# Performance work log

Measured on AMD Instinct MI355X. Metric: run time of the kernel, lower is better.

The kernel has to match this reference:

```python
import jax, jax.numpy as jnp
import numpy as np

B_GR = 128    # graphs per batch
N0 = 512      # nodes per graph before pooling
E_PER = 4096  # edges per graph (kept static; pooled-away edges get weight 0)
H = 128       # hidden
F = 128       # num_features (== hidden)
C = 10        # num_classes
K_HOP = 3     # Jacobi polynomial order (hop_num)
A_J, B_J = 1.0, 1.0
EPS = 1e-5


def _bn(h, g, b):
    # training-mode BatchNorm1d: batch stats, biased variance
    m = jnp.mean(h, 0)
    v = jnp.mean((h - m) ** 2, 0)
    return (h - m) * jax.lax.rsqrt(v + EPS) * g + b


def _forward(x, convW, convb, bnW, bnB, bn7W, bn7B, attW, theta,
             lin1W, lin1b, lin2W, lin2b, lin3W, lin3b, src, dst):
    w = jnp.ones((src.shape[0],), x.dtype)  # edge weights; 0 => filtered edge
    n = N0
    h = x
    reads = []
    for i in range(5):
        N = B_GR * n
        # symmetric GCN normalization with self loops on the weighted graph
        deg = jax.ops.segment_sum(w, dst, num_segments=N) + 1.0
        dinv = jax.lax.rsqrt(deg)
        enorm = dinv[src] * dinv[dst] * w   # per-edge norm [E]
        snorm = dinv * dinv                 # self-loop norm [N]
        prop = lambda m_: jax.ops.segment_sum(enorm[:, None] * m_[src], dst, num_segments=N) + m_ * snorm[:, None]
        pvec = lambda v_: jax.ops.segment_sum(enorm * v_[src], dst, num_segments=N) + v_ * snorm
        # GCNConv -> BN -> ReLU
        h = prop(h @ convW[i]) + convb[i]
        h = jax.nn.relu(_bn(h, bnW[i], bnB[i]))
        # JacobiPool: Jacobi-polynomial diffusion of attention scores
        s0 = h @ attW[i]                    # [N]
        polys = [s0, 0.5 * ((A_J - B_J) * s0 + (A_J + B_J + 2.0) * pvec(s0))]
        for kk in range(2, K_HOP + 1):
            c0 = 2 * kk * (kk + A_J + B_J) * (2 * kk + A_J + B_J - 2)
            c1 = (2 * kk + A_J + B_J - 1) * (2 * kk + A_J + B_J) * (2 * kk + A_J + B_J - 2)
            c2 = (2 * kk + A_J + B_J - 1) * (A_J * A_J - B_J * B_J)
            c3 = 2 * (kk + A_J - 1) * (kk + B_J - 1) * (2 * kk + A_J + B_J)
            polys.append((c1 * pvec(polys[-1]) + c2 * polys[-1] - c3 * polys[-2]) / c0)
        score = sum(theta[i, j] * polys[j] for j in range(K_HOP + 1))
        # top-k node selection per graph (ratio 0.5 -> static k)
        k = n // 2
        _, idx = jax.lax.top_k(score.reshape(B_GR, n), k)
        sel = (idx + (jnp.arange(B_GR) * n)[:, None]).reshape(-1)  # global node ids [B*k]
        h = h[sel] * jnp.tanh(score[sel])[:, None]
        # remap/filter edges to surviving nodes (masked, static edge count)
        new_id = jnp.full((N,), -1, jnp.int32).at[sel].set(jnp.arange(B_GR * k, dtype=jnp.int32))
        ns, nd = new_id[src], new_id[dst]
        valid = (ns >= 0) & (nd >= 0) & (w > 0)
        w = valid.astype(x.dtype)
        src = jnp.where(valid, ns, 0)
        dst = jnp.where(valid, nd, 0)
        # readout: global max pool || global mean pool per graph
        xg = h.reshape(B_GR, k, H)
        reads.append(jnp.concatenate([xg.max(1), xg.mean(1)], -1))
        n = k
    g = sum(reads) / 5.0                    # [B, 2H]
    g = jax.nn.relu(_bn(g @ lin1W + lin1b, bnW[5], bnB[5]))
    g = jax.nn.relu(_bn(g @ lin2W + lin2b, bn7W, bn7B))
    return jax.nn.log_softmax(g @ lin3W + lin3b, -1)


def setup_inputs() -> dict:
    key = jax.random.key(0)
    ks = jax.random.split(key, 8)
    N = B_GR * N0
    E = B_GR * E_PER
    rng = np.random.default_rng(0)
    off = np.repeat(np.arange(B_GR, dtype=np.int32) * N0, E_PER)
    src = jnp.asarray(off + rng.integers(0, N0, E).astype(np.int32))
    dst = jnp.asarray(off + rng.integers(0, N0, E).astype(np.int32))
    s = 1.0 / np.sqrt(H)
    return {
        "x": jax.random.normal(ks[0], (N, F), jnp.float32),
        "convW": jax.random.normal(ks[1], (5, H, H), jnp.float32) * s,
        "convb": jnp.zeros((5, H), jnp.float32),
        "bnW": jnp.ones((6, H), jnp.float32),
        "bnB": jnp.zeros((6, H), jnp.float32),
        "bn7W": jnp.ones((H // 2,), jnp.float32),
        "bn7B": jnp.zeros((H // 2,), jnp.float32),
        "attW": jax.random.normal(ks[2], (5, H), jnp.float32) * s,
        "theta": jax.random.normal(ks[3], (5, K_HOP + 1), jnp.float32) * 0.5,
        "lin1W": jax.random.normal(ks[4], (2 * H, H), jnp.float32) * (1.0 / np.sqrt(2 * H)),
        "lin1b": jnp.zeros((H,), jnp.float32),
        "lin2W": jax.random.normal(ks[5], (H, H // 2), jnp.float32) * s,
        "lin2b": jnp.zeros((H // 2,), jnp.float32),
        "lin3W": jax.random.normal(ks[6], (H // 2, C), jnp.float32) * (1.0 / np.sqrt(H // 2)),
        "lin3b": jnp.zeros((C,), jnp.float32),
        "src": src,
        "dst": dst,
    }


def reference(x, convW, convb, bnW, bnB, bn7W, bn7B, attW, theta,
              lin1W, lin1b, lin2W, lin2b, lin3W, lin3b, src, dst):
    return _forward(x, convW, convb, bnW, bnB, bn7W, bn7B, attW, theta,
                    lin1W, lin1b, lin2W, lin2b, lin3W, lin3b, src, dst)
```

## Files before the change

kernel.cpp:

```cpp
#include <hip/hip_runtime.h>
#include <hip/hip_bf16.h>

#define B_GRAPH 128
#define ETOT    (128*4096)
#define N0G     (128*512)
#define HF      128
#define STSZ    2048

union IGSmem {
    float Ws[64*HF];
    struct { int cnt[512]; int cur[512]; float dvl[512]; } ini;
};

__global__ __launch_bounds__(256) void k_init_gemm(
    const float* __restrict__ A, const float* __restrict__ Wg, float* __restrict__ C,
    const int* __restrict__ s_in, const int* __restrict__ d_in_,
    int* __restrict__ srcw, int* __restrict__ dstw, float* __restrict__ wv,
    int2* __restrict__ csr, int2* __restrict__ rb2, float* __restrict__ dinvv,
    float* __restrict__ gacc, float* __restrict__ statsH,
    float* __restrict__ st0, float* __restrict__ st1, float* __restrict__ st2)
{
    __shared__ IGSmem sm;
    int t = threadIdx.x;
    if (blockIdx.x < 1024){
        int tx = t & 15, ty = t >> 4;
        int r0 = blockIdx.x*64 + ty*4, c0 = tx*4;
        float acc[4][8];
        #pragma unroll
        for (int j=0;j<4;++j)
            #pragma unroll
            for (int l=0;l<8;++l) acc[j][l] = 0.f;
        for (int kh = 0; kh < 2; ++kh){
            __syncthreads();
            {
                float4* d4 = (float4*)sm.Ws;
                const float4* s4 = (const float4*)(Wg + kh*64*HF);
                for (int i = t; i < 64*HF/4; i += 256) d4[i] = s4[i];
            }
            __syncthreads();
            for (int k4 = 0; k4 < 16; ++k4){
                float4 av[4];
                #pragma unroll
                for (int j=0;j<4;++j)
                    av[j] = *(const float4*)(A + (size_t)(r0+j)*HF + kh*64 + k4*4);
                #pragma unroll
                for (int kk=0; kk<4; ++kk){
                    int kl = k4*4 + kk;
                    float4 w0 = *(const float4*)(sm.Ws + kl*HF + c0);
                    float4 w1 = *(const float4*)(sm.Ws + kl*HF + c0 + 64);
                    #pragma unroll
                    for (int j=0;j<4;++j){
                        float a = reinterpret_cast<const float*>(&av[j])[kk];
                        acc[j][0] += a*w0.x; acc[j][1] += a*w0.y; acc[j][2] += a*w0.z; acc[j][3] += a*w0.w;
                        acc[j][4] += a*w1.x; acc[j][5] += a*w1.y; acc[j][6] += a*w1.z; acc[j][7] += a*w1.w;
                    }
                }
            }
        }
        #pragma unroll
        for (int j=0;j<4;++j){
            *(float4*)(C + (size_t)(r0+j)*HF + c0)      = make_float4(acc[j][0],acc[j][1],acc[j][2],acc[j][3]);
            *(float4*)(C + (size_t)(r0+j)*HF + c0 + 64) = make_float4(acc[j][4],acc[j][5],acc[j][6],acc[j][7]);
        }
    } else {
        int g = blockIdx.x - 1024;
        for (int l = t; l < 512; l += 256) sm.ini.cnt[l] = 0;
        gacc[g*256 + t] = 0.f;
        if (g == 0){
            if (t < 256){ statsH[t] = 0.f; if (t < 128) statsH[256+t] = 0.f; }
            for (int i = t; i < STSZ; i += 256){ st0[i] = 0.f; st1[i] = 0.f; st2[i] = 0.f; }
        }
        __syncthreads();
        for (int j = t; j < 4096; j += 256){
            int e = g*4096 + j;
            int sg = s_in[e], dg = d_in_[e];
            srcw[e] = sg; dstw[e] = dg; wv[e] = 1.f;
            atomicAdd(&sm.ini.cnt[dg & 511], 1);
        }
        __syncthreads();
        int c0 = sm.ini.cnt[2*t], c1 = sm.ini.cnt[2*t+1];
        int pairsum = c0 + c1;
        sm.ini.cur[t] = pairsum;
        __syncthreads();
        for (int off = 1; off < 256; off <<= 1){
            int a = (t >= off) ? sm.ini.cur[t-off] : 0;
            __syncthreads();
            sm.ini.cur[t] += a;
            __syncthreads();
        }
        int begpair = sm.ini.cur[t] - pairsum;
        __syncthreads();
        sm.ini.cur[2*t]   = begpair;
        sm.ini.cur[2*t+1] = begpair + c0;
        __syncthreads();
        for (int l = t; l < 512; l += 256){
            rb2[g*512 + l] = make_int2(g*4096 + sm.ini.cur[l], sm.ini.cnt[l]);
            float dv = rsqrtf((float)sm.ini.cnt[l] + 1.f);
            sm.ini.dvl[l] = dv;
            dinvv[g*512 + l] = dv;
        }
        __syncthreads();
        for (int j = t; j < 4096; j += 256){
            int e = g*4096 + j;
            int sg = srcw[e], dl = dstw[e] & 511;
            int p = atomicAdd(&sm.ini.cur[dl], 1);
            csr[g*4096 + p] = make_int2(sg, __float_as_int(sm.ini.dvl[sg & 511]));
        }
    }
}

__global__ __launch_bounds__(256) void k_prop_stats(const float* __restrict__ Y, const float* __restrict__ cb,
                                                    const int2* __restrict__ rb2, const int2* __restrict__ cp,
                                                    const float* __restrict__ dinv,
                                                    float* __restrict__ X, float* __restrict__ st,
                                                    int n, int lb, int Nn){
    __shared__ float rs[1024], rq[1024];
    int xcd = blockIdx.x & 7, c = blockIdx.x >> 3;
    int g = xcd*16 + (c >> lb);
    int m = c & ((1 << lb) - 1);
    int nd = threadIdx.x >> 5;
    int v = g*n + m*8 + nd;
    int f4 = threadIdx.x & 31;
    float dv = dinv[v];
    float4 y = *(const float4*)(Y + (size_t)v*HF + f4*4);
    float4 acc = make_float4(0.f, 0.f, 0.f, 0.f);
    int2 rb = rb2[v];
    int e0 = rb.x, e1 = rb.x + rb.y;
    for (int j = e0; j < e1; ++j){
        int2 e = cp[j];
        int s = e.x & (Nn - 1);
        float en = __int_as_float(e.y);
        float4 h = *(const float4*)(Y + (size_t)s*HF + f4*4);
        acc.x += en*h.x; acc.y += en*h.y; acc.z += en*h.z; acc.w += en*h.w;
    }
    int f = f4*4;
    acc.x = y.x*dv*dv + dv*acc.x + cb[f];
    acc.y = y.y*dv*dv + dv*acc.y + cb[f+1];
    acc.z = y.z*dv*dv + dv*acc.z + cb[f+2];
    acc.w = y.w*dv*dv + dv*acc.w + cb[f+3];
    *(float4*)(X + (size_t)v*HF + f) = acc;
    *(float4*)&rs[nd*HF + f] = acc;
    *(float4*)&rq[nd*HF + f] = make_float4(acc.x*acc.x, acc.y*acc.y, acc.z*acc.z, acc.w*acc.w);
    __syncthreads();
    if (threadIdx.x < 128){
        int tt = threadIdx.x;
        float s = 0.f, q = 0.f;
        #pragma unroll
        for (int j = 0; j < 8; ++j){ s += rs[j*HF + tt]; q += rq[j*HF + tt]; }
        atomicAdd(&st[xcd*256 + tt], s);
        atomicAdd(&st[xcd*256 + 128 + tt], q);
    }
}

union __align__(16) KSmem {
    struct {
        int2  eds[4096]; int2 rbl[512];
        float dvv[512], p0[512], p1[512], p2[512];
        float ss[512]; int si[512]; float tss[256]; int nid[512];
        int   cntN[256], curN[256]; float dvn[256];
        float bna[128], bnb[128]; float red[1024]; float awl[128];
    } gr;
    struct { float Ws[64*HF]; float red[32*HF]; } cv;
};

__global__ __launch_bounds__(1024) void k_graph(
    const float* __restrict__ H, const float* __restrict__ stats,
    const float* __restrict__ gw, const float* __restrict__ gb,
    const float* __restrict__ aw, const float* __restrict__ th,
    const int2* __restrict__ rb2, int2* __restrict__ csr, const float* __restrict__ dinv,
    int* __restrict__ srcw, int* __restrict__ dstw, float* __restrict__ wv,
    float* __restrict__ P, float* __restrict__ gacc,
    int2* __restrict__ rb2n, float* __restrict__ dinvn,
    float* __restrict__ stZero, float* __restrict__ stAcc,
    const float* __restrict__ Wnext, const float* __restrict__ cbNext,
    float* __restrict__ Gnext, float* __restrict__ Hnext,
    const float* __restrict__ lin1W, const float* __restrict__ lin1b,
    float* __restrict__ t1g, float* __restrict__ statsH,
    float invN, float ca2, float cc2, float ca3, float cc3,
    int n, int last)
{
    int g = blockIdx.x, t = threadIdx.x;
    int k = n >> 1;
    __shared__ KSmem sm;

    if (t < 256) stZero[(g & 7)*256 + t] = 0.f;
    if (t < 128){
        float s = 0.f, q = 0.f;
        #pragma unroll
        for (int b2 = 0; b2 < 8; ++b2){ s += stats[b2*256 + t]; q += stats[b2*256 + 128 + t]; }
        float mean = s*invN;
        float var  = q*invN - mean*mean;
        float iv   = rsqrtf(var + 1e-5f);
        sm.gr.bna[t] = iv*gw[t];
        sm.gr.bnb[t] = gb[t] - mean*iv*gw[t];
        sm.gr.awl[t] = aw[t];
    }
    for (int l = t; l < n; l += 1024){
        int2 rb = rb2[g*n + l];
        sm.gr.rbl[l] = make_int2(rb.x - g*4096, rb.y);
        sm.gr.dvv[l] = dinv[g*n + l];
    }
    __syncthreads();
    int medg = sm.gr.rbl[n-1].x + sm.gr.rbl[n-1].y;
    for (int j = t; j < medg; j += 1024){
        int2 e = csr[g*4096 + j];
        sm.gr.eds[j] = make_int2(e.x & (n-1), e.y);
    }
    {
        int l = t >> 1, h = t & 1;
        float part = 0.f;
        if (l < n){
            const float* hp = H + ((size_t)g*n + l)*HF + h*64;
            #pragma unroll
            for (int j = 0; j < 16; ++j){
                float4 v = *(const float4*)(hp + j*4);
                int f = h*64 + j*4;
                float4 a4 = *(const float4*)&sm.gr.bna[f];
                float4 b4 = *(const float4*)&sm.gr.bnb[f];
                float4 w4 = *(const float4*)&sm.gr.awl[f];
                part += fmaxf(v.x*a4.x + b4.x, 0.f)*w4.x
                      + fmaxf(v.y*a4.y + b4.y, 0.f)*w4.y
                      + fmaxf(v.z*a4.z + b4.z, 0.f)*w4.z
                      + fmaxf(v.w*a4.w + b4.w, 0.f)*w4.w;
            }
        }
        sm.gr.red[t] = part;
    }
    __syncthreads();
    for (int l = t; l < n; l += 1024) sm.gr.p0[l] = sm.gr.red[2*l] + sm.gr.red[2*l+1];
    __syncthreads();
    for (int l = t; l < n; l += 1024){
        int2 rc = sm.gr.rbl[l];
        float acc = 0.f;
        for (int j = 0; j < rc.y; ++j){
            int2 e = sm.gr.eds[rc.x + j];
            acc += __int_as_float(e.y) * sm.gr.p0[e.x];
        }
        float dv = sm.gr.dvv[l];
        sm.gr.p1[l] = 2.f*(sm.gr.p0[l]*dv*dv + dv*acc);
    }
    __syncthreads();
    for (int l = t; l < n; l += 1024){
        int2 rc = sm.gr.rbl[l];
        float acc = 0.f;
        for (int j = 0; j < rc.y; ++j){
            int2 e = sm.gr.eds[rc.x + j];
            acc += __int_as_float(e.y) * sm.gr.p1[e.x];
        }
        float dv = sm.gr.dvv[l];
        sm.gr.p2[l] = ca2*(sm.gr.p1[l]*dv*dv + dv*acc) + cc2*sm.gr.p0[l];
    }
    __syncthreads();
    float t0v = th[0], t1v = th[1], t2c = th[2], t3v = th[3];
    for (int l = t; l < n; l += 1024){
        int2 rc = sm.gr.rbl[l];
        float acc = 0.f;
        for (int j = 0; j < rc.y; ++j){
            int2 e = sm.gr.eds[rc.x + j];
            acc += __int_as_float(e.y) * sm.gr.p2[e.x];
        }
        float dv = sm.gr.dvv[l];
        float tv = sm.gr.p2[l]*dv*dv + dv*acc;
        float p3 = ca3*tv + cc3*sm.gr.p1[l];
        sm.gr.ss[l] = t0v*sm.gr.p0[l] + t1v*sm.gr.p1[l] + t2c*sm.gr.p2[l] + t3v*p3;
        sm.gr.si[l] = l;
    }
    __syncthreads();
    for (int size = 2; size <= n; size <<= 1){
        for (int stride = size >> 1; stride > 0; stride >>= 1){
            for (int i = t; i < n; i += 1024){
                int j = i ^ stride;
                if (j > i){
                    bool asc = ((i & size) == 0);
                    float s1 = sm.gr.ss[i], s2 = sm.gr.ss[j];
                    int   i1 = sm.gr.si[i], i2 = sm.gr.si[j];
                    bool gt = (s1 < s2) || (s1 == s2 && i1 > i2);
                    if (gt == asc){ sm.gr.ss[i] = s2; sm.gr.ss[j] = s1; sm.gr.si[i] = i2; sm.gr.si[j] = i1; }
                }
            }
            __syncthreads();
        }
    }
    for (int l = t; l < n; l += 1024) sm.gr.nid[l] = -1;
    __syncthreads();
    for (int r = t; r < k; r += 1024){
        sm.gr.nid[sm.gr.si[r]] = r;
        sm.gr.tss[r] = tanhf(sm.gr.ss[r]);
    }
    __syncthreads();
    {
        int f4 = t & 31, rl = t >> 5;
        int f = f4*4;
        float4 a4 = *(const float4*)&sm.gr.bna[f];
        float4 b4 = *(const float4*)&sm.gr.bnb[f];
        float4 mx = make_float4(-3.4e38f,-3.4e38f,-3.4e38f,-3.4e38f);
        float4 smv = make_float4(0.f,0.f,0.f,0.f);
        for (int r = rl; r < k; r += 32){
            int old = sm.gr.si[r];
            float4 hv = *(const float4*)(H + ((size_t)g*n + old)*HF + f);
            float ts = sm.gr.tss[r];
            float4 v;
            v.x = fmaxf(hv.x*a4.x + b4.x, 0.f)*ts;
            v.y = fmaxf(hv.y*a4.y + b4.y, 0.f)*ts;
            v.z = fmaxf(hv.z*a4.z + b4.z, 0.f)*ts;
            v.w = fmaxf(hv.w*a4.w + b4.w, 0.f)*ts;
            *(float4*)(P + ((size_t)g*k + r)*HF + f) = v;
            mx.x = fmaxf(mx.x, v.x); mx.y = fmaxf(mx.y, v.y);
            mx.z = fmaxf(mx.z, v.z); mx.w = fmaxf(mx.w, v.w);
            smv.x += v.x; smv.y += v.y; smv.z += v.z; smv.w += v.w;
        }
        float* scr = (float*)sm.gr.eds;
        *(float4*)&scr[rl*128 + f]        = mx;
        *(float4*)&scr[4096 + rl*128 + f] = smv;
        __syncthreads();
        if (t < 128){
            float m = -3.4e38f, s = 0.f;
            #pragma unroll
            for (int j = 0; j < 32; ++j){
                m = fmaxf(m, scr[j*128 + t]);
                s += scr[4096 + j*128 + t];
            }
            gacc[g*256 + t] += m;
            gacc[g*256 + 128 + t] += s / (float)k;
        }
    }
    if (last){
        __syncthreads();
        int c = t & 127, h = t >> 7;
        float s = 0.f;
        int k0 = h*32;
        #pragma unroll
        for (int kk = 0; kk < 32; ++kk)
            s += gacc[g*256 + k0 + kk] * lin1W[(k0 + kk)*128 + c];
        sm.gr.red[t] = s;
        __syncthreads();
        if (t < 512) sm.gr.red[t] += sm.gr.red[t+512];
        __syncthreads();
        if (t < 256) sm.gr.red[t] += sm.gr.red[t+256];
        __syncthreads();
        if (t < 128){
            float v = (sm.gr.red[t] + sm.gr.red[t+128]) * 0.2f + lin1b[t];
            t1g[g*128 + t] = v;
            atomicAdd(&statsH[t], v);
            atomicAdd(&statsH[128+t], v*v);
        }
        return;
    }
    __syncthreads();
    if (t < k) sm.gr.cntN[t] = 0;
    __syncthreads();
    for (int j = t; j < 4096; j += 1024){
        int e = g*4096 + j;
        float we = wv[e];
        int valid = 0, ns = 0, nd = 0;
        if (we > 0.5f){
            int sl = srcw[e] & (n-1);
            int dl = dstw[e] & (n-1);
            ns = sm.gr.nid[sl]; nd = sm.gr.nid[dl];
            valid = (ns >= 0) && (nd >= 0);
        }
        if (valid){
            srcw[e] = g*k + ns; dstw[e] = g*k + nd; wv[e] = 1.f;
            atomicAdd(&sm.gr.cntN[nd], 1);
        } else {
            srcw[e] = 0; dstw[e] = 0; wv[e] = 0.f;
        }
    }
    __syncthreads();
    int c = (t < 256) ? ((t < k) ? sm.gr.cntN[t] : 0) : 0;
    if (t < 256) sm.gr.si[t] = c;
    __syncthreads();
    for (int off = 1; off < 256; off <<= 1){
        int a = 0;
        if (t < 256 && t >= off) a = sm.gr.si[t-off];
        __syncthreads();
        if (t < 256) sm.gr.si[t] += a;
        __syncthreads();
    }
    if (t < k){
        int beg = sm.gr.si[t] - c;
        rb2n[g*k + t] = make_int2(g*4096 + beg, c);
        float dv = rsqrtf((float)c + 1.f);
        dinvn[g*k + t] = dv;
        sm.gr.dvn[t] = dv;
        sm.gr.curN[t] = beg;
    }
    __syncthreads();
    for (int j = t; j < 4096; j += 1024){
        int e = g*4096 + j;
        if (wv[e] > 0.5f){
            int sg = srcw[e], dl = dstw[e] & (k-1);
            int p = atomicAdd(&sm.gr.curN[dl], 1);
            csr[g*4096 + p] = make_int2(sg, __float_as_int(sm.gr.dvn[sg & (k-1)]));
        }
    }
    __syncthreads();
    int Nn2 = B_GRAPH * k;
    {
        int sub = t >> 8, t8 = t & 255, tx = t8 & 15, ty = t8 >> 4;
        int cc0 = tx*4;
        int nT = (k + 255) >> 8;
        for (int tile = 0; tile < nT; ++tile){
            int r0 = tile*256 + sub*64 + ty*4;
            bool act = (r0 < k);
            float acc[4][8];
            #pragma unroll
            for (int j=0;j<4;++j)
                #pragma unroll
                for (int l=0;l<8;++l) acc[j][l] = 0.f;
            for (int kh = 0; kh < 2; ++kh){
                __syncthreads();
                {
                    float4* d4 = (float4*)sm.cv.Ws;
                    const float4* s4 = (const float4*)(Wnext + kh*64*HF);
                    #pragma unroll
                    for (int i2 = 0; i2 < 2; ++i2) d4[t + i2*1024] = s4[t + i2*1024];
                }
                __syncthreads();
                if (act){
                    for (int k4 = 0; k4 < 16; ++k4){
                        float4 av[4];
                        #pragma unroll
                        for (int j=0;j<4;++j)
                            av[j] = *(const float4*)(P + ((size_t)g*k + r0 + j)*HF + kh*64 + k4*4);
                        #pragma unroll
                        for (int kk=0; kk<4; ++kk){
                            int kl = k4*4 + kk;
                            float4 w0 = *(const float4*)(sm.cv.Ws + kl*HF + cc0);
                            float4 w1 = *(const float4*)(sm.cv.Ws + kl*HF + cc0 + 64);
                            #pragma unroll
                            for (int j=0;j<4;++j){
                                float aa = reinterpret_cast<const float*>(&av[j])[kk];
                                acc[j][0] += aa*w0.x; acc[j][1] += aa*w0.y; acc[j][2] += aa*w0.z; acc[j][3] += aa*w0.w;
                                acc[j][4] += aa*w1.x; acc[j][5] += aa*w1.y; acc[j][6] += aa*w1.z; acc[j][7] += aa*w1.w;
                            }
                        }
                    }
                }
            }
            if (act){
                #pragma unroll
                for (int j=0;j<4;++j){
                    *(float4*)(Gnext + ((size_t)g*k + r0 + j)*HF + cc0)      = make_float4(acc[j][0],acc[j][1],acc[j][2],acc[j][3]);
                    *(float4*)(Gnext + ((size_t)g*k + r0 + j)*HF + cc0 + 64) = make_float4(acc[j][4],acc[j][5],acc[j][6],acc[j][7]);
                }
            }
        }
    }
    __syncthreads();
    {
        int f = (t & 31)*4;
        float4 s  = make_float4(0.f,0.f,0.f,0.f);
        float4 s2 = make_float4(0.f,0.f,0.f,0.f);
        float cb0 = cbNext[f], cb1 = cbNext[f+1], cb2 = cbNext[f+2], cb3 = cbNext[f+3];
        for (int l = t >> 5; l < k; l += 32){
            int v = g*k + l;
            float dv = dinvn[v];
            float4 y = *(const float4*)(Gnext + (size_t)v*HF + f);
            float4 acc = make_float4(0.f,0.f,0.f,0.f);
            int2 rb = rb2n[v];
            int e1 = rb.x + rb.y;
            for (int j = rb.x; j < e1; ++j){
                int2 e = csr[j];
                int sN = e.x & (Nn2 - 1);
                float en = __int_as_float(e.y);
                float4 h = *(const float4*)(Gnext + (size_t)sN*HF + f);
                acc.x += en*h.x; acc.y += en*h.y; acc.z += en*h.z; acc.w += en*h.w;
            }
            acc.x = y.x*dv*dv + dv*acc.x + cb0;
            acc.y = y.y*dv*dv + dv*acc.y + cb1;
            acc.z = y.z*dv*dv + dv*acc.z + cb2;
            acc.w = y.w*dv*dv + dv*acc.w + cb3;
            *(float4*)(Hnext + (size_t)v*HF + f) = acc;
            s.x += acc.x; s.y += acc.y; s.z += acc.z; s.w += acc.w;
            s2.x += acc.x*acc.x; s2.y += acc.y*acc.y; s2.z += acc.z*acc.z; s2.w += acc.w*acc.w;
        }
        int base = (t >> 5)*HF + f;
        __syncthreads();
        *(float4*)&sm.cv.red[base] = s;
        __syncthreads();
        if (t < 128){
            float a = 0.f;
            #pragma unroll
            for (int j = 0; j < 32; ++j) a += sm.cv.red[j*HF + t];
            atomicAdd(&stAcc[(g & 7)*256 + t], a);
        }
        __syncthreads();
        *(float4*)&sm.cv.red[base] = s2;
        __syncthreads();
        if (t < 128){
            float a = 0.f;
            #pragma unroll
            for (int j = 0; j < 32; ++j) a += sm.cv.red[j*HF + t];
            atomicAdd(&stAcc[(g & 7)*256 + 128 + t], a);
        }
    }
}

__global__ __launch_bounds__(128) void k_head2(const float* __restrict__ t1, const float* __restrict__ gw,
                                               const float* __restrict__ gb, const float* __restrict__ W2,
                                               const float* __restrict__ b2, float* __restrict__ sh,
                                               float* __restrict__ t2){
    int r = blockIdx.x, t = threadIdx.x;
    int cc = t & 63, h = t >> 6;
    __shared__ float row[128];
    __shared__ float red[128];
    {
        float mean = sh[t] * (1.f/128.f);
        float var  = sh[128+t]*(1.f/128.f) - mean*mean;
        float iv   = rsqrtf(var + 1e-5f);
        float v = (t1[r*128+t] - mean)*iv*gw[t] + gb[t];
        row[t] = fmaxf(v, 0.f);
    }
    __syncthreads();
    float s = 0.f;
    #pragma unroll
    for (int kk = 0; kk < 64; ++kk)
        s += row[h*64+kk] * W2[(h*64+kk)*64 + cc];
    red[t] = s;
    __syncthreads();
    if (h == 0){
        float v = red[cc] + red[cc+64] + b2[cc];
        t2[r*64+cc] = v;
        atomicAdd(&sh[256+cc], v);
        atomicAdd(&sh[320+cc], v*v);
    }
}
__global__ __launch_bounds__(64) void k_head3(const float* __restrict__ t2, const float* __restrict__ gw,
                                              const float* __restrict__ gb, const float* __restrict__ W3,
                                              const float* __restrict__ b3, const float* __restrict__ sh,
                                              float* __restrict__ out){
    int r = blockIdx.x, t = threadIdx.x;
    float mean = sh[256+t]*(1.f/128.f);
    float var  = sh[320+t]*(1.f/128.f) - mean*mean;
    float iv   = rsqrtf(var + 1e-5f);
    float v = fmaxf((t2[r*64+t]-mean)*iv*gw[t] + gb[t], 0.f);
    float lg[10];
    #pragma unroll
    for (int j = 0; j < 10; ++j){
        float p = v * W3[t*10 + j];
        for (int off = 32; off; off >>= 1) p += __shfl_down(p, off);
        lg[j] = p;
    }
    if (t == 0){
        float m = -3.4e38f;
        #pragma unroll
        for (int j = 0; j < 10; ++j){ lg[j] += b3[j]; m = fmaxf(m, lg[j]); }
        float se = 0.f;
        #pragma unroll
        for (int j = 0; j < 10; ++j) se += expf(lg[j] - m);
        float l = logf(se) + m;
        #pragma unroll
        for (int j = 0; j < 10; ++j) out[r*10 + j] = lg[j] - l;
    }
}

extern "C" void kernel_launch(void* const* d_in, const int* in_sizes, int n_in,
                              void* d_out, int out_size, void* d_ws, size_t ws_size,
                              hipStream_t stream){
    const float* x     = (const float*)d_in[0];
    const float* convW = (const float*)d_in[1];
    const float* convb = (const float*)d_in[2];
    const float* bnW   = (const float*)d_in[3];
    const float* bnB   = (const float*)d_in[4];
    const float* bn7W  = (const float*)d_in[5];
    const float* bn7B  = (const float*)d_in[6];
    const float* attW  = (const float*)d_in[7];
    const float* theta = (const float*)d_in[8];
    const float* lin1W = (const float*)d_in[9];
    const float* lin1b = (const float*)d_in[10];
    const float* lin2W = (const float*)d_in[11];
    const float* lin2b = (const float*)d_in[12];
    const float* lin3W = (const float*)d_in[13];
    const float* lin3b = (const float*)d_in[14];
    const int*   src0  = (const int*)d_in[15];
    const int*   dst0  = (const int*)d_in[16];

    char* base = (char*)d_ws;
    size_t off = 0;
    auto take = [&](size_t bytes) -> void* {
        void* p = base + off;
        off = (off + bytes + 255) & ~(size_t)255;
        return p;
    };
    float* bufGP = (float*)take((size_t)N0G*HF*4);
    float* bufHA = (float*)take((size_t)N0G*HF*4);
    float* bufHB = (float*)take((size_t)(N0G/2)*HF*4);
    int*   srcw  = (int*)  take((size_t)ETOT*4);
    int*   dstw  = (int*)  take((size_t)ETOT*4);
    float* w     = (float*)take((size_t)ETOT*4);
    int2*  csr_p = (int2*) take((size_t)ETOT*8);
    int2*  rb2A  = (int2*) take((size_t)N0G*8);
    int2*  rb2B  = (int2*) take((size_t)N0G*8);
    float* dinvA = (float*)take((size_t)N0G*4);
    float* dinvB = (float*)take((size_t)N0G*4);
    float* st[3];
    st[0] = (float*)take(STSZ*4);
    st[1] = (float*)take(STSZ*4);
    st[2] = (float*)take(STSZ*4);
    float* gacc  = (float*)take((size_t)B_GRAPH*256*4);
    float* t1    = (float*)take((size_t)B_GRAPH*128*4);
    float* t2    = (float*)take((size_t)B_GRAPH*64*4);
    float* statsH= (float*)take(384*4);

    auto coef = [](int kk, float& ca, float& cc){
        double a = 1.0, b = 1.0;
        double c0 = 2.0*kk*(kk+a+b)*(2.0*kk+a+b-2.0);
        double c1 = (2.0*kk+a+b-1.0)*(2.0*kk+a+b)*(2.0*kk+a+b-2.0);
        double c3 = 2.0*(kk+a-1.0)*(kk+b-1.0)*(2.0*kk+a+b);
        ca = (float)(c1/c0); cc = (float)(-c3/c0);
    };
    float ca2, cc2, ca3, cc3;
    coef(2, ca2, cc2);
    coef(3, ca3, cc3);

    k_init_gemm<<<1024 + B_GRAPH, 256, 0, stream>>>(x, convW, bufGP,
                                                    src0, dst0, srcw, dstw, w, csr_p, rb2A, dinvA,
                                                    gacc, statsH, st[0], st[1], st[2]);
    k_prop_stats<<<N0G/8, 256, 0, stream>>>(bufGP, convb, rb2A, csr_p, dinvA, bufHA, st[0], 512, 6, N0G);

    float* G = bufGP + (size_t)4*1024*1024;

    for (int i = 0; i < 5; ++i){
        int n = 512 >> i;
        int Nn = B_GRAPH*n;
        int2*  rb_cur = (i & 1) ? rb2B : rb2A;
        int2*  rb_nxt = (i & 1) ? rb2A : rb2B;
        float* dv_cur = (i & 1) ? dinvB : dinvA;
        float* dv_nxt = (i & 1) ? dinvA : dinvB;
        float* Hcur = (i & 1) ? bufHB : bufHA;
        float* Hnxt = (i & 1) ? bufHA : bufHB;
        int wnext = (i < 4) ? (i + 1) : 4;

        k_graph<<<B_GRAPH, 1024, 0, stream>>>(Hcur, st[i % 3], bnW + i*HF, bnB + i*HF, attW + i*HF,
                                              theta + i*4, rb_cur, csr_p, dv_cur,
                                              srcw, dstw, w, bufGP, gacc, rb_nxt, dv_nxt,
                                              st[(i + 2) % 3], st[(i + 1) % 3],
                                              convW + (size_t)wnext*HF*HF, convb + wnext*HF,
                                              G, Hnxt,
                                              lin1W, lin1b, t1, statsH,
                                              1.0f/(float)Nn, ca2, cc2, ca3, cc3, n, (i == 4) ? 1 : 0);
    }

    k_head2<<<B_GRAPH, 128, 0, stream>>>(t1, bnW + 5*HF, bnB + 5*HF, lin2W, lin2b, statsH, t2);
    k_head3<<<B_GRAPH, 64, 0, stream>>>(t2, bn7W, bn7B, lin3W, lin3b, statsH, (float*)d_out);
}
```

Baseline: 403.2 us.

## Split per-graph GEMM and propagation into grid-wide kernels; rank-count top-k

The next-layer GEMM and GCN propagation with BN-stat accumulation move out of the per-graph k_graph kernel, which ran only 128 blocks. They now run as a standalone tiled k_gemm and the existing k_prop_stats kernel, each launched over all rows for more parallelism across CUs. The bitonic sort used for top-k is replaced by an O(n^2) rank count per node in shared memory, which removes the many barrier-separated sort passes. This costs two extra launches per layer and a global round-trip for the pooled features.

```diff
diff --git a/kernel.cpp b/kernel.cpp
--- a/kernel.cpp
+++ b/kernel.cpp
@@ -152,7 +152,53 @@
     }
 }
 
-union __align__(16) KSmem {
+__global__ __launch_bounds__(256) void k_gemm(const float* __restrict__ A, const float* __restrict__ Wg,
+                                              float* __restrict__ C)
+{
+    __shared__ float Ws[64*HF];
+    int t = threadIdx.x;
+    int tx = t & 15, ty = t >> 4;
+    int r0 = blockIdx.x*64 + ty*4, c0 = tx*4;
+    float acc[4][8];
+    #pragma unroll
+    for (int j=0;j<4;++j)
+        #pragma unroll
+        for (int l=0;l<8;++l) acc[j][l] = 0.f;
+    for (int kh = 0; kh < 2; ++kh){
+        __syncthreads();
+        {
+            float4* d4 = (float4*)Ws;
+            const float4* s4 = (const float4*)(Wg + kh*64*HF);
+            for (int i = t; i < 64*HF/4; i += 256) d4[i] = s4[i];
+        }
+        __syncthreads();
+        for (int k4 = 0; k4 < 16; ++k4){
+            float4 av[4];
+            #pragma unroll
+            for (int j=0;j<4;++j)
+                av[j] = *(const float4*)(A + (size_t)(r0+j)*HF + kh*64 + k4*4);
+            #pragma unroll
+            for (int kk=0; kk<4; ++kk){
+                int kl = k4*4 + kk;
+                float4 w0 = *(const float4*)(Ws + kl*HF + c0);
+                float4 w1 = *(const float4*)(Ws + kl*HF + c0 + 64);
+                #pragma unroll
+                for (int j=0;j<4;++j){
+                    float a = reinterpret_cast<const float*>(&av[j])[kk];
+                    acc[j][0] += a*w0.x; acc[j][1] += a*w0.y; acc[j][2] += a*w0.z; acc[j][3] += a*w0.w;
+                    acc[j][4] += a*w1.x; acc[j][5] += a*w1.y; acc[j][6] += a*w1.z; acc[j][7] += a*w1.w;
+                }
+            }
+        }
+    }
+    #pragma unroll
+    for (int j=0;j<4;++j){
+        *(float4*)(C + (size_t)(r0+j)*HF + c0)      = make_float4(acc[j][0],acc[j][1],acc[j][2],acc[j][3]);
+        *(float4*)(C + (size_t)(r0+j)*HF + c0 + 64) = make_float4(acc[j][4],acc[j][5],acc[j][6],acc[j][7]);
+    }
+}
+
+struct __align__(16) KSmem {
     struct {
         int2  eds[4096]; int2 rbl[512];
         float dvv[512], p0[512], p1[512], p2[512];
@@ -160,7 +206,6 @@
         int   cntN[256], curN[256]; float dvn[256];
         float bna[128], bnb[128]; float red[1024]; float awl[128];
     } gr;
-    struct { float Ws[64*HF]; float red[32*HF]; } cv;
 };
 
 __global__ __launch_bounds__(1024) void k_graph(
@@ -171,9 +216,7 @@
     int* __restrict__ srcw, int* __restrict__ dstw, float* __restrict__ wv,
     float* __restrict__ P, float* __restrict__ gacc,
     int2* __restrict__ rb2n, float* __restrict__ dinvn,
-    float* __restrict__ stZero, float* __restrict__ stAcc,
-    const float* __restrict__ Wnext, const float* __restrict__ cbNext,
-    float* __restrict__ Gnext, float* __restrict__ Hnext,
+    float* __restrict__ stZero,
     const float* __restrict__ lin1W, const float* __restrict__ lin1b,
     float* __restrict__ t1g, float* __restrict__ statsH,
     float invN, float ca2, float cc2, float ca3, float cc3,
@@ -263,29 +306,25 @@
         float tv = sm.gr.p2[l]*dv*dv + dv*acc;
         float p3 = ca3*tv + cc3*sm.gr.p1[l];
         sm.gr.ss[l] = t0v*sm.gr.p0[l] + t1v*sm.gr.p1[l] + t2c*sm.gr.p2[l] + t3v*p3;
-        sm.gr.si[l] = l;
-    }
-    __syncthreads();
-    for (int size = 2; size <= n; size <<= 1){
-        for (int stride = size >> 1; stride > 0; stride >>= 1){
-            for (int i = t; i < n; i += 1024){
-                int j = i ^ stride;
-                if (j > i){
-                    bool asc = ((i & size) == 0);
-                    float s1 = sm.gr.ss[i], s2 = sm.gr.ss[j];
-                    int   i1 = sm.gr.si[i], i2 = sm.gr.si[j];
-                    bool gt = (s1 < s2) || (s1 == s2 && i1 > i2);
-                    if (gt == asc){ sm.gr.ss[i] = s2; sm.gr.ss[j] = s1; sm.gr.si[i] = i2; sm.gr.si[j] = i1; }
-                }
-            }
-            __syncthreads();
-        }
-    }
-    for (int l = t; l < n; l += 1024) sm.gr.nid[l] = -1;
-    __syncthreads();
-    for (int r = t; r < k; r += 1024){
-        sm.gr.nid[sm.gr.si[r]] = r;
-        sm.gr.tss[r] = tanhf(sm.gr.ss[r]);
+    }
+    __syncthreads();
+    for (int l = t; l < n; l += 1024){
+        float sl = sm.gr.ss[l];
+        int r = 0;
+        for (int j = 0; j < n; j += 4){
+            float4 s4 = *(const float4*)&sm.gr.ss[j];
+            r += (s4.x > sl) || (s4.x == sl && (j    ) < l);
+            r += (s4.y > sl) || (s4.y == sl && (j + 1) < l);
+            r += (s4.z > sl) || (s4.z == sl && (j + 2) < l);
+            r += (s4.w > sl) || (s4.w == sl && (j + 3) < l);
+        }
+        if (r < k){
+            sm.gr.nid[l] = r;
+            sm.gr.si[r]  = l;
+            sm.gr.tss[r] = tanhf(sl);
+        } else {
+            sm.gr.nid[l] = -1;
+        }
     }
     __syncthreads();
     {
@@ -392,107 +431,6 @@
             int sg = srcw[e], dl = dstw[e] & (k-1);
             int p = atomicAdd(&sm.gr.curN[dl], 1);
             csr[g*4096 + p] = make_int2(sg, __float_as_int(sm.gr.dvn[sg & (k-1)]));
-        }
-    }
-    __syncthreads();
-    int Nn2 = B_GRAPH * k;
-    {
-        int sub = t >> 8, t8 = t & 255, tx = t8 & 15, ty = t8 >> 4;
-        int cc0 = tx*4;
-        int nT = (k + 255) >> 8;
-        for (int tile = 0; tile < nT; ++tile){
-            int r0 = tile*256 + sub*64 + ty*4;
-            bool act = (r0 < k);
-            float acc[4][8];
-            #pragma unroll
-            for (int j=0;j<4;++j)
-                #pragma unroll
-                for (int l=0;l<8;++l) acc[j][l] = 0.f;
-            for (int kh = 0; kh < 2; ++kh){
-                __syncthreads();
-                {
-                    float4* d4 = (float4*)sm.cv.Ws;
-                    const float4* s4 = (const float4*)(Wnext + kh*64*HF);
-                    #pragma unroll
-                    for (int i2 = 0; i2 < 2; ++i2) d4[t + i2*1024] = s4[t + i2*1024];
-                }
-                __syncthreads();
-                if (act){
-                    for (int k4 = 0; k4 < 16; ++k4){
-                        float4 av[4];
-                        #pragma unroll
-                        for (int j=0;j<4;++j)
-                            av[j] = *(const float4*)(P + ((size_t)g*k + r0 + j)*HF + kh*64 + k4*4);
-                        #pragma unroll
-                        for (int kk=0; kk<4; ++kk){
-                            int kl = k4*4 + kk;
-                            float4 w0 = *(const float4*)(sm.cv.Ws + kl*HF + cc0);
-                            float4 w1 = *(const float4*)(sm.cv.Ws + kl*HF + cc0 + 64);
-                            #pragma unroll
-                            for (int j=0;j<4;++j){
-                                float aa = reinterpret_cast<const float*>(&av[j])[kk];
-                                acc[j][0] += aa*w0.x; acc[j][1] += aa*w0.y; acc[j][2] += aa*w0.z; acc[j][3] += aa*w0.w;
-                                acc[j][4] += aa*w1.x; acc[j][5] += aa*w1.y; acc[j][6] += aa*w1.z; acc[j][7] += aa*w1.w;
-                            }
-                        }
-                    }
-                }
-            }
-            if (act){
-                #pragma unroll
-                for (int j=0;j<4;++j){
-                    *(float4*)(Gnext + ((size_t)g*k + r0 + j)*HF + cc0)      = make_float4(acc[j][0],acc[j][1],acc[j][2],acc[j][3]);
-                    *(float4*)(Gnext + ((size_t)g*k + r0 + j)*HF + cc0 + 64) = make_float4(acc[j][4],acc[j][5],acc[j][6],acc[j][7]);
-                }
-            }
-        }
-    }
-    __syncthreads();
-    {
-        int f = (t & 31)*4;
-        float4 s  = make_float4(0.f,0.f,0.f,0.f);
-        float4 s2 = make_float4(0.f,0.f,0.f,0.f);
-        float cb0 = cbNext[f], cb1 = cbNext[f+1], cb2 = cbNext[f+2], cb3 = cbNext[f+3];
-        for (int l = t >> 5; l < k; l += 32){
-            int v = g*k + l;
-            float dv = dinvn[v];
-            float4 y = *(const float4*)(Gnext + (size_t)v*HF + f);
-            float4 acc = make_float4(0.f,0.f,0.f,0.f);
-            int2 rb = rb2n[v];
-            int e1 = rb.x + rb.y;
-            for (int j = rb.x; j < e1; ++j){
-                int2 e = csr[j];
-                int sN = e.x & (Nn2 - 1);
-                float en = __int_as_float(e.y);
-                float4 h = *(const float4*)(Gnext + (size_t)sN*HF + f);
-                acc.x += en*h.x; acc.y += en*h.y; acc.z += en*h.z; acc.w += en*h.w;
-            }
-            acc.x = y.x*dv*dv + dv*acc.x + cb0;
-            acc.y = y.y*dv*dv + dv*acc.y + cb1;
-            acc.z = y.z*dv*dv + dv*acc.z + cb2;
-            acc.w = y.w*dv*dv + dv*acc.w + cb3;
-            *(float4*)(Hnext + (size_t)v*HF + f) = acc;
-            s.x += acc.x; s.y += acc.y; s.z += acc.z; s.w += acc.w;
-            s2.x += acc.x*acc.x; s2.y += acc.y*acc.y; s2.z += acc.z*acc.z; s2.w += acc.w*acc.w;
-        }
-        int base = (t >> 5)*HF + f;
-        __syncthreads();
-        *(float4*)&sm.cv.red[base] = s;
-        __syncthreads();
-        if (t < 128){
-            float a = 0.f;
-            #pragma unroll
-            for (int j = 0; j < 32; ++j) a += sm.cv.red[j*HF + t];
-            atomicAdd(&stAcc[(g & 7)*256 + t], a);
-        }
-        __syncthreads();
-        *(float4*)&sm.cv.red[base] = s2;
-        __syncthreads();
-        if (t < 128){
-            float a = 0.f;
-            #pragma unroll
-            for (int j = 0; j < 32; ++j) a += sm.cv.red[j*HF + t];
-            atomicAdd(&stAcc[(g & 7)*256 + 128 + t], a);
         }
     }
 }
@@ -623,6 +561,7 @@
 
     for (int i = 0; i < 5; ++i){
         int n = 512 >> i;
+        int kk = n >> 1;
         int Nn = B_GRAPH*n;
         int2*  rb_cur = (i & 1) ? rb2B : rb2A;
         int2*  rb_nxt = (i & 1) ? rb2A : rb2B;
@@ -630,16 +569,21 @@
         float* dv_nxt = (i & 1) ? dinvA : dinvB;
         float* Hcur = (i & 1) ? bufHB : bufHA;
         float* Hnxt = (i & 1) ? bufHA : bufHB;
-        int wnext = (i < 4) ? (i + 1) : 4;
 
         k_graph<<<B_GRAPH, 1024, 0, stream>>>(Hcur, st[i % 3], bnW + i*HF, bnB + i*HF, attW + i*HF,
                                               theta + i*4, rb_cur, csr_p, dv_cur,
                                               srcw, dstw, w, bufGP, gacc, rb_nxt, dv_nxt,
-                                              st[(i + 2) % 3], st[(i + 1) % 3],
-                                              convW + (size_t)wnext*HF*HF, convb + wnext*HF,
-                                              G, Hnxt,
+                                              st[(i + 1) % 3],
                                               lin1W, lin1b, t1, statsH,
                                               1.0f/(float)Nn, ca2, cc2, ca3, cc3, n, (i == 4) ? 1 : 0);
+        if (i < 4){
+            int wnext = i + 1;
+            int rows = B_GRAPH * kk;
+            k_gemm<<<rows/64, 256, 0, stream>>>(bufGP, convW + (size_t)wnext*HF*HF, G);
+            int lbn = (kk == 256) ? 5 : (kk == 128) ? 4 : (kk == 64) ? 3 : 2;
+            k_prop_stats<<<rows/8, 256, 0, stream>>>(G, convb + wnext*HF, rb_nxt, csr_p, dv_nxt,
+                                                     Hnxt, st[(i + 1) % 3], kk, lbn, rows);
+        }
     }
 
     k_head2<<<B_GRAPH, 128, 0, stream>>>(t1, bnW + 5*HF, bnB + 5*HF, lin2W, lin2b, statsH, t2);
```

After: 407.7 us. No clear change (+1.1%).
